# Optimization experiments

Measured on AMD Instinct MI355X. Metric: run time of the kernel, lower is better.

The kernel has to match this reference:

```python
import jax, jax.numpy as jnp
import numpy as np

S = 72
IMG_W, IMG_H = 640, 360
STRIDE = 32
FMAP_H, FMAP_W = IMG_H // STRIDE, IMG_W // STRIDE  # 11, 20
N_OFFSETS = S
N_STRIPS = S - 1
ANGLES = np.array([15.0, 22.0, 30.0, 39.0, 49.0, 60.0, 72.0, 80.0, 90.0, 100.0, 108.0, 120.0, 131.0, 141.0, 150.0, 158.0, 165.0])
N_ANG = 17
N_PRED = 2 + 2 + 1 + N_OFFSETS  # 77
N_EDGE = FMAP_W + 2 * FMAP_H    # 42
N_PROP = N_ANG * N_EDGE         # 714
NMS_THRES = 15.0
BACKBONE_C = 512
CONV_C = 1024


def _make_anchors():
    anchor_ys = np.linspace(1.0, 0.0, N_OFFSETS)
    tan = np.tan(np.deg2rad(ANGLES))
    def side(origins):
        out = np.zeros((N_ANG, N_PRED, len(origins)), np.float32)
        for i, (sx, sy) in enumerate(origins):
            out[:, 2, i] = 1.0 - sy
            out[:, 3, i] = sx
            out[:, 5:, i] = (sx + (sy - anchor_ys)[None, :] / tan[:, None]) * IMG_W
        return out.reshape(N_ANG * N_PRED, len(origins))
    left = side([(0.0, y) for y in np.linspace(1.0, 0.0, FMAP_H)])
    right = side([(1.0, y) for y in np.linspace(1.0, 0.0, FMAP_H)])
    bottom = side([(x, 1.0) for x in np.linspace(1.0, 0.0, FMAP_W)])
    anchors = np.zeros((N_ANG * N_PRED, FMAP_H, FMAP_W), np.float32)
    anchors[:, :, 0] = left
    anchors[:, :, -1] = right
    anchors[:, -1, :] = bottom
    edge = np.concatenate([anchors[:, :, 0], anchors[:, :, -1], anchors[:, -1, :]], 1)  # [1309,42]
    anch_dim = edge.reshape(N_ANG, N_PRED, N_EDGE).transpose(2, 0, 1).reshape(N_PROP, N_PRED)
    return jnp.asarray(anchors), jnp.asarray(anch_dim)


def setup_inputs():
    key = jax.random.key(0)
    ks = jax.random.split(key, 4)
    B = 32
    feat = jax.random.normal(ks[0], (B, BACKBONE_C, FMAP_H, FMAP_W), jnp.float32)
    W_conv = jax.random.normal(ks[1], (CONV_C, BACKBONE_C), jnp.float32) * 0.02
    b_conv = jnp.zeros((CONV_C,), jnp.float32)
    W_cls = jax.random.normal(ks[2], (2 * N_ANG, CONV_C), jnp.float32) * 0.02
    b_cls = jnp.zeros((2 * N_ANG,), jnp.float32)
    W_reg = jax.random.normal(ks[3], (N_ANG * (N_OFFSETS + 1), CONV_C), jnp.float32) * 0.02
    b_reg = jnp.zeros((N_ANG * (N_OFFSETS + 1),), jnp.float32)
    anchors, anchors_anchor_dim = _make_anchors()
    return {"feat": feat, "W_conv": W_conv, "b_conv": b_conv, "W_cls": W_cls, "b_cls": b_cls,
            "W_reg": W_reg, "b_reg": b_reg, "anchors": anchors, "anchors_anchor_dim": anchors_anchor_dim}


def _proposals(feat, W_conv, b_conv, W_cls, b_cls, W_reg, b_reg, anchors):
    B = feat.shape[0]
    features = jnp.einsum('bchw,oc->bohw', feat, W_conv) + b_conv[None, :, None, None]
    cls_f = jnp.einsum('bchw,oc->bohw', features, W_cls) + b_cls[None, :, None, None]
    reg_f = jnp.einsum('bchw,oc->bohw', features, W_reg) + b_reg[None, :, None, None]
    anch = anchors.reshape(N_ANG, N_PRED, FMAP_H, FMAP_W)
    cls_r = cls_f.reshape(B, N_ANG, 2, FMAP_H, FMAP_W)
    reg_r = reg_f.reshape(B, N_ANG, N_OFFSETS + 1, FMAP_H, FMAP_W)
    # slots 0:2 <- cls logits (set), slots 2:4 <- anchor (copied), slots 4: <- anchor + reg
    mid = jnp.broadcast_to(anch[None, :, 2:4], (B, N_ANG, 2, FMAP_H, FMAP_W))
    tail = anch[None, :, 4:] + reg_r
    lane = jnp.concatenate([cls_r, mid, tail], axis=2)  # [B,17,77,h,w]
    # gather the three feature-map edges: left col, right col, bottom row
    edges = jnp.concatenate([lane[:, :, :, :, 0], lane[:, :, :, :, -1], lane[:, :, :, -1, :]], axis=3)  # [B,17,77,42]
    return edges.transpose(0, 3, 1, 2).reshape(B, N_PROP, N_PRED)  # [B,714,77]


def _nms_one(props, scores):
    # greedy line-NMS over proposals of one image, shapes static
    order = jnp.argsort(-scores)
    p = props[order]
    start = jnp.clip(jnp.round(p[:, 2] * N_STRIPS), 0.0, float(N_STRIPS))
    end = jnp.clip(start + p[:, 4] - 1.0, 0.0, float(N_STRIPS))
    xs = p[:, 5:]  # [N,72]
    s = jnp.maximum(start[:, None], start[None, :])
    e = jnp.minimum(end[:, None], end[None, :])
    idx = jnp.arange(N_OFFSETS, dtype=p.dtype)
    m = (idx[None, None, :] >= s[..., None]) & (idx[None, None, :] <= e[..., None])  # [N,N,72]
    diff = jnp.abs(xs[:, None, :] - xs[None, :, :])  # [N,N,72]
    cnt = e - s + 1.0
    dist = jnp.where(cnt > 0, jnp.sum(diff * m, -1) / jnp.maximum(cnt, 1.0), jnp.inf)
    sup = dist < NMS_THRES
    n = p.shape[0]
    pos = jnp.arange(n)
    def step(suppressed, i):
        keep_i = ~suppressed[i]
        suppressed = suppressed | (keep_i & sup[i] & (pos > i))
        return suppressed, keep_i
    _, keep_sorted = jax.lax.scan(step, jnp.zeros(n, bool), pos)
    return jnp.zeros(n, bool).at[order].set(keep_sorted)


def reference(feat, W_conv, b_conv, W_cls, b_cls, W_reg, b_reg, anchors, anchors_anchor_dim):
    proposals = _proposals(feat, W_conv, b_conv, W_cls, b_cls, W_reg, b_reg, anchors)
    scores = jax.nn.softmax(proposals[..., :2], axis=-1)[..., 1]  # [B,714]
    keep_mask = jax.lax.map(lambda pr: _nms_one(pr[0], pr[1]), (proposals, scores))  # [B,714]
    return proposals, keep_mask, scores
```

## Files before the change

kernel.cpp:

```cpp
#include <hip/hip_runtime.h>
#include <math.h>

#define NB     32
#define FH     11
#define FW     20
#define CIN    512
#define CMID   1024
#define NANG   17
#define NPREDD 77
#define NEDGE  42
#define NPROPP 714
#define NOFF   72
#define NCLS   34
#define NREGR  1241
#define N2PAD  1280
#define MTOT   1344
#define NSTRIPSF 71.0f
#define PADK   40

typedef unsigned long long u64;
typedef unsigned short ushortt;
typedef short s8v __attribute__((ext_vector_type(8)));
typedef ushortt u4v __attribute__((ext_vector_type(4)));
typedef float f4v __attribute__((ext_vector_type(4)));

__device__ inline ushortt f2bf(float f) {
    unsigned u = __float_as_uint(f);
    u += 0x7fffu + ((u >> 16) & 1u);
    return (ushortt)(u >> 16);
}
__device__ inline float bf2f(ushortt h) {
    return __uint_as_float(((unsigned)h) << 16);
}

__global__ __launch_bounds__(256) void k_prep(const float* __restrict__ feat,
                                              ushortt* __restrict__ A1hi,
                                              ushortt* __restrict__ A1lo,
                                              const float* __restrict__ Wconv,
                                              ushortt* __restrict__ B1h,
                                              ushortt* __restrict__ B1l,
                                              const float* __restrict__ Wcls,
                                              const float* __restrict__ Wreg,
                                              ushortt* __restrict__ B2h,
                                              ushortt* __restrict__ B2l)
{
    __shared__ unsigned T[32 * 221];
    int bid = blockIdx.x, tid = threadIdx.x;
    if (bid < 512) {
        int p0 = bid * 32;
        int b  = p0 >> 9;
        int c0 = p0 & 511;
        const float* fp = feat + (size_t)p0 * 220;
        for (int i = tid; i < 32 * 220; i += 256) {
            float v = fp[i];
            int pl = i / 220, off = i - pl * 220;
            ushortt hi = f2bf(v);
            ushortt lo = f2bf(v - bf2f(hi));
            T[pl * 221 + off] = ((unsigned)hi) | (((unsigned)lo) << 16);
        }
        __syncthreads();
        int cl = tid & 31;
        for (int e = tid >> 5; e < NEDGE; e += 8) {
            int hw = (e < FH) ? e * FW
                   : (e < 2 * FH) ? (e - FH) * FW + (FW - 1)
                   : (FH - 1) * FW + (e - 2 * FH);
            unsigned u = T[cl * 221 + hw];
            size_t o = (size_t)(b * NEDGE + e) * CIN + c0 + cl;
            A1hi[o] = (ushortt)(u & 0xffffu);
            A1lo[o] = (ushortt)(u >> 16);
        }
    } else if (bid < 1024) {
        int t = (bid - 512) * 256 + tid;
        float4 v = *(const float4*)(Wconv + (size_t)t * 4);
        float vf[4] = {v.x, v.y, v.z, v.w};
        u4v hv, lv;
#pragma unroll
        for (int j = 0; j < 4; ++j) {
            ushortt h = f2bf(vf[j]);
            hv[j] = h;
            lv[j] = f2bf(vf[j] - bf2f(h));
        }
        *(u4v*)(B1h + (size_t)t * 4) = hv;
        *(u4v*)(B1l + (size_t)t * 4) = lv;
    } else {
        int t = (bid - 1024) * 256 + tid;
        int row = t >> 8, col = (t & 255) * 4;
        float4 v = make_float4(0.f, 0.f, 0.f, 0.f);
        if (row < NCLS)              v = *(const float4*)(Wcls + (size_t)row * CMID + col);
        else if (row < NCLS + NREGR) v = *(const float4*)(Wreg + (size_t)(row - NCLS) * CMID + col);
        float vf[4] = {v.x, v.y, v.z, v.w};
        u4v hv, lv;
#pragma unroll
        for (int j = 0; j < 4; ++j) {
            ushortt h = f2bf(vf[j]);
            hv[j] = h;
            lv[j] = f2bf(vf[j] - bf2f(h));
        }
        *(u4v*)(B2h + (size_t)t * 4) = hv;
        *(u4v*)(B2l + (size_t)t * 4) = lv;
    }
}

__global__ __launch_bounds__(256) void k_gemm1m(const ushortt* __restrict__ Ahi,
                                                const ushortt* __restrict__ Alo,
                                                const ushortt* __restrict__ Bh,
                                                const ushortt* __restrict__ Bl,
                                                const float* __restrict__ bias,
                                                ushortt* __restrict__ Chi,
                                                ushortt* __restrict__ Clo)
{
    const int K = CIN, N = CMID;
    __shared__ __align__(16) ushortt Ash[2][64 * PADK], Asl[2][64 * PADK];
    __shared__ __align__(16) ushortt Bsh[2][64 * PADK], Bsl[2][64 * PADK];
    int tid = threadIdx.x;
    int m0 = blockIdx.y * 64, n0 = blockIdx.x * 64;
    int srow = tid >> 2, sg = tid & 3;
    int lane = tid & 63, wv = tid >> 6;
    int wm = (wv & 1) * 32, wn = (wv >> 1) * 32;
    int quad = lane >> 4, l15 = lane & 15;
    int wo = srow * PADK + sg * 8;

    f4v acc[2][2];
#pragma unroll
    for (int i = 0; i < 2; ++i)
#pragma unroll
        for (int j = 0; j < 2; ++j) acc[i][j] = (f4v){0.f, 0.f, 0.f, 0.f};

    const ushortt* Ahp = Ahi + (size_t)(m0 + srow) * K + sg * 8;
    const ushortt* Alp = Alo + (size_t)(m0 + srow) * K + sg * 8;
    const ushortt* Bhp = Bh  + (size_t)(n0 + srow) * K + sg * 8;
    const ushortt* Blp = Bl  + (size_t)(n0 + srow) * K + sg * 8;

    s8v ra = *(const s8v*)Ahp;
    s8v rl = *(const s8v*)Alp;
    s8v rb = *(const s8v*)Bhp;
    s8v rc = *(const s8v*)Blp;
    *(s8v*)&Ash[0][wo] = ra;
    *(s8v*)&Asl[0][wo] = rl;
    *(s8v*)&Bsh[0][wo] = rb;
    *(s8v*)&Bsl[0][wo] = rc;
    __syncthreads();

    int buf = 0;
    for (int k0 = 0; k0 < K; k0 += 32) {
        bool more = (k0 + 32 < K);
        if (more) {
            ra = *(const s8v*)(Ahp + k0 + 32);
            rl = *(const s8v*)(Alp + k0 + 32);
            rb = *(const s8v*)(Bhp + k0 + 32);
            rc = *(const s8v*)(Blp + k0 + 32);
        }
        s8v ah[2], al[2], bh[2], bl[2];
#pragma unroll
        for (int s = 0; s < 2; ++s) {
            ah[s] = *(const s8v*)&Ash[buf][(wm + s * 16 + l15) * PADK + quad * 8];
            al[s] = *(const s8v*)&Asl[buf][(wm + s * 16 + l15) * PADK + quad * 8];
            bh[s] = *(const s8v*)&Bsh[buf][(wn + s * 16 + l15) * PADK + quad * 8];
            bl[s] = *(const s8v*)&Bsl[buf][(wn + s * 16 + l15) * PADK + quad * 8];
        }
#pragma unroll
        for (int sm = 0; sm < 2; ++sm)
#pragma unroll
            for (int sn = 0; sn < 2; ++sn) {
                acc[sm][sn] = __builtin_amdgcn_mfma_f32_16x16x32_bf16(al[sm], bl[sn], acc[sm][sn], 0, 0, 0);
                acc[sm][sn] = __builtin_amdgcn_mfma_f32_16x16x32_bf16(al[sm], bh[sn], acc[sm][sn], 0, 0, 0);
                acc[sm][sn] = __builtin_amdgcn_mfma_f32_16x16x32_bf16(ah[sm], bl[sn], acc[sm][sn], 0, 0, 0);
                acc[sm][sn] = __builtin_amdgcn_mfma_f32_16x16x32_bf16(ah[sm], bh[sn], acc[sm][sn], 0, 0, 0);
            }
        if (more) {
            *(s8v*)&Ash[buf ^ 1][wo] = ra;
            *(s8v*)&Asl[buf ^ 1][wo] = rl;
            *(s8v*)&Bsh[buf ^ 1][wo] = rb;
            *(s8v*)&Bsl[buf ^ 1][wo] = rc;
        }
        __syncthreads();
        buf ^= 1;
    }
#pragma unroll
    for (int sm = 0; sm < 2; ++sm)
#pragma unroll
        for (int sn = 0; sn < 2; ++sn)
#pragma unroll
            for (int r = 0; r < 4; ++r) {
                int m = m0 + wm + sm * 16 + quad * 4 + r;
                int n = n0 + wn + sn * 16 + l15;
                float v = acc[sm][sn][r] + bias[n];
                ushortt h = f2bf(v);
                Chi[(size_t)m * N + n] = h;
                Clo[(size_t)m * N + n] = f2bf(v - bf2f(h));
            }
}

__global__ __launch_bounds__(256) void k_gemm2m(const ushortt* __restrict__ Ahi,
                                                const ushortt* __restrict__ Alo,
                                                const ushortt* __restrict__ Bh,
                                                const ushortt* __restrict__ Bl,
                                                const float* __restrict__ bcls,
                                                const float* __restrict__ breg,
                                                float* __restrict__ C)
{
    const int K = CMID;
    __shared__ __align__(16) ushortt Ash[2][64 * PADK], Asl[2][64 * PADK];
    __shared__ __align__(16) ushortt Bsh[2][64 * PADK], Bsl[2][64 * PADK];
    int tid = threadIdx.x;
    int m0 = blockIdx.y * 64, n0 = blockIdx.x * 64;
    int srow = tid >> 2, sg = tid & 3;
    int lane = tid & 63, wv = tid >> 6;
    int wm = (wv & 1) * 32, wn = (wv >> 1) * 32;
    int quad = lane >> 4, l15 = lane & 15;
    int wo = srow * PADK + sg * 8;

    f4v acc[2][2];
#pragma unroll
    for (int i = 0; i < 2; ++i)
#pragma unroll
        for (int j = 0; j < 2; ++j) acc[i][j] = (f4v){0.f, 0.f, 0.f, 0.f};

    const ushortt* Ahp = Ahi + (size_t)(m0 + srow) * K + sg * 8;
    const ushortt* Alp = Alo + (size_t)(m0 + srow) * K + sg * 8;
    const ushortt* Bhp = Bh  + (size_t)(n0 + srow) * K + sg * 8;
    const ushortt* Blp = Bl  + (size_t)(n0 + srow) * K + sg * 8;

    s8v ra = *(const s8v*)Ahp;
    s8v rl = *(const s8v*)Alp;
    s8v rb = *(const s8v*)Bhp;
    s8v rc = *(const s8v*)Blp;
    *(s8v*)&Ash[0][wo] = ra;
    *(s8v*)&Asl[0][wo] = rl;
    *(s8v*)&Bsh[0][wo] = rb;
    *(s8v*)&Bsl[0][wo] = rc;
    __syncthreads();

    int buf = 0;
    for (int k0 = 0; k0 < K; k0 += 32) {
        bool more = (k0 + 32 < K);
        if (more) {
            ra = *(const s8v*)(Ahp + k0 + 32);
            rl = *(const s8v*)(Alp + k0 + 32);
            rb = *(const s8v*)(Bhp + k0 + 32);
            rc = *(const s8v*)(Blp + k0 + 32);
        }
        s8v ah[2], al[2], bh[2], bl[2];
#pragma unroll
        for (int s = 0; s < 2; ++s) {
            ah[s] = *(const s8v*)&Ash[buf][(wm + s * 16 + l15) * PADK + quad * 8];
            al[s] = *(const s8v*)&Asl[buf][(wm + s * 16 + l15) * PADK + quad * 8];
            bh[s] = *(const s8v*)&Bsh[buf][(wn + s * 16 + l15) * PADK + quad * 8];
            bl[s] = *(const s8v*)&Bsl[buf][(wn + s * 16 + l15) * PADK + quad * 8];
        }
#pragma unroll
        for (int sm = 0; sm < 2; ++sm)
#pragma unroll
            for (int sn = 0; sn < 2; ++sn) {
                acc[sm][sn] = __builtin_amdgcn_mfma_f32_16x16x32_bf16(al[sm], bl[sn], acc[sm][sn], 0, 0, 0);
                acc[sm][sn] = __builtin_amdgcn_mfma_f32_16x16x32_bf16(al[sm], bh[sn], acc[sm][sn], 0, 0, 0);
                acc[sm][sn] = __builtin_amdgcn_mfma_f32_16x16x32_bf16(ah[sm], bl[sn], acc[sm][sn], 0, 0, 0);
                acc[sm][sn] = __builtin_amdgcn_mfma_f32_16x16x32_bf16(ah[sm], bh[sn], acc[sm][sn], 0, 0, 0);
            }
        if (more) {
            *(s8v*)&Ash[buf ^ 1][wo] = ra;
            *(s8v*)&Asl[buf ^ 1][wo] = rl;
            *(s8v*)&Bsh[buf ^ 1][wo] = rb;
            *(s8v*)&Bsl[buf ^ 1][wo] = rc;
        }
        __syncthreads();
        buf ^= 1;
    }
#pragma unroll
    for (int sm = 0; sm < 2; ++sm)
#pragma unroll
        for (int sn = 0; sn < 2; ++sn)
#pragma unroll
            for (int r = 0; r < 4; ++r) {
                int m = m0 + wm + sm * 16 + quad * 4 + r;
                int n = n0 + wn + sn * 16 + l15;
                float bb = (n < NCLS) ? bcls[n] : ((n < NCLS + NREGR) ? breg[n - NCLS] : 0.f);
                C[(size_t)m * N2PAD + n] = acc[sm][sn][r] + bb;
            }
}

__global__ __launch_bounds__(256) void k_assemble(const float* __restrict__ C2,
                                                  const float* __restrict__ AD,
                                                  float* __restrict__ outP,
                                                  float* __restrict__ outS,
                                                  float* __restrict__ startv,
                                                  float* __restrict__ endv,
                                                  float* __restrict__ xsel)
{
    int mb = blockIdx.x;
    int b = mb / NEDGE, e = mb - b * NEDGE;
    const float* c2 = C2 + (size_t)mb * N2PAD;
    int tid = threadIdx.x;
    for (int idx = tid; idx < NANG * NPREDD; idx += 256) {
        int a = idx / NPREDD, p = idx - a * NPREDD;
        int prop = e * NANG + a;
        float v;
        if (p < 2) v = c2[a * 2 + p];
        else {
            v = AD[prop * NPREDD + p];
            if (p >= 4) v += c2[NCLS + a * 73 + (p - 4)];
        }
        outP[((size_t)b * NPROPP + prop) * NPREDD + p] = v;
    }
    if (tid < NANG) {
        int a = tid, prop = e * NANG + a;
        float c0 = c2[2 * a], c1 = c2[2 * a + 1];
        float mx = fmaxf(c0, c1);
        float e0 = expf(c0 - mx), e1 = expf(c1 - mx);
        outS[b * NPROPP + prop] = e1 / (e0 + e1);
        float p2 = AD[prop * NPREDD + 2];
        float p4 = AD[prop * NPREDD + 4] + c2[NCLS + a * 73];
        float st = fminf(fmaxf(rintf(p2 * NSTRIPSF), 0.0f), NSTRIPSF);
        float en = fminf(fmaxf(st + p4 - 1.0f, 0.0f), NSTRIPSF);
        startv[b * 720 + prop] = st;
        endv[b * 720 + prop] = en;
        int ksi = (int)st;
        xsel[b * 720 + prop] = AD[prop * NPREDD + 5 + ksi] + c2[NCLS + a * 73 + ksi + 1];
    }
}

__global__ __launch_bounds__(128) void k_sort(const float* __restrict__ scores,
                                              int* __restrict__ order)
{
    int b = blockIdx.x, tile = blockIdx.y, tid = threadIdx.x;
    __shared__ __align__(16) float s[720];
    for (int x = tid; x < 720; x += 128)
        s[x] = (x < NPROPP) ? scores[b * NPROPP + x] : -1e30f;
    __syncthreads();
    int i = tile * 128 + tid;
    if (i >= NPROPP) return;
    float si = s[i];
    int r = 0;
#pragma unroll 4
    for (int j4 = 0; j4 < 720; j4 += 4) {
        float4 v = *(const float4*)&s[j4];
        r += (v.x > si) || (v.x == si && (j4 + 0) < i);
        r += (v.y > si) || (v.y == si && (j4 + 1) < i);
        r += (v.z > si) || (v.z == si && (j4 + 2) < i);
        r += (v.w > si) || (v.w == si && (j4 + 3) < i);
    }
    order[b * 720 + r] = i;
}

__global__ __launch_bounds__(256) void k_supmat(const float* __restrict__ outP,
                                                const float* __restrict__ startv,
                                                const float* __restrict__ endv,
                                                const float* __restrict__ xsel,
                                                const int* __restrict__ order,
                                                u64* __restrict__ sup)
{
    int jt = blockIdx.x, it = blockIdx.y, b = blockIdx.z;
    int i0 = it * 64, j0 = jt * 64;
    int tid = threadIdx.x;
    if (j0 + 63 < i0) {
        if (tid < 64) {
            int il = i0 + tid;
            if (il < NPROPP) sup[((size_t)b * NPROPP + il) * 12 + jt] = 0ull;
        }
        return;
    }
    __shared__ float SI[64], EI[64], XI[64];
    __shared__ float SJ[64], EJ[64], XJ[64];
    __shared__ int   OI[64], OJ[64];
    if (tid < 128) {
        int side = tid >> 6, q = tid & 63;
        int pos = (side ? j0 : i0) + q;
        int o = (pos < NPROPP) ? order[b * 720 + pos] : -1;
        float st = (o >= 0) ? startv[b * 720 + o] : 0.f;
        float en = (o >= 0) ? endv[b * 720 + o] : -2.f;
        float xv = (o >= 0) ? xsel[b * 720 + o] : 0.f;
        if (!side) { SI[q] = st; EI[q] = en; XI[q] = xv; OI[q] = o; }
        else       { SJ[q] = st; EJ[q] = en; XJ[q] = xv; OJ[q] = o; }
    }
    __syncthreads();
    int lane = tid & 63, w = tid >> 6;
    int j = j0 + lane;
    float sj = SJ[lane], ej = EJ[lane], xj = XJ[lane];
    const float* basexs = outP + (size_t)b * NPROPP * NPREDD + 5;
#pragma unroll 1
    for (int rep = 0; rep < 16; ++rep) {
        int iloc = w * 16 + rep;
        int il = i0 + iloc;
        float si = SI[iloc], ei = EI[iloc];
        float s = fmaxf(si, sj), e = fminf(ei, ej);
        float cnt = e - s + 1.0f;
        bool sp = false;
        if (cnt > 0.f) {
            if (e < s) {
                sp = true;
            } else {
                int ks = (int)s, ke = (int)e;
                if (si == sj && ke == ks) {
                    sp = (fabsf(XI[iloc] - xj) / fmaxf(cnt, 1.0f)) < 15.0f;
                } else {
                    const float* xi  = basexs + (size_t)OI[iloc] * NPREDD;
                    const float* xjp = basexs + (size_t)OJ[lane] * NPREDD;
                    float sum = 0.f;
                    for (int k = ks; k <= ke; ++k)
                        sum += fabsf(xi[k] - xjp[k]);
                    sp = (sum / fmaxf(cnt, 1.0f)) < 15.0f;
                }
            }
        }
        bool valid = (il < NPROPP) && (j < NPROPP) && (j > il);
        u64 msk = __ballot(valid && sp);
        if (lane == 0 && il < NPROPP)
            sup[((size_t)b * NPROPP + il) * 12 + jt] = msk;
    }
}

__global__ __launch_bounds__(256) void k_scan(const u64* __restrict__ sup,
                                              const int* __restrict__ order,
                                              float* __restrict__ keep_out)
{
    int b = blockIdx.x, tid = threadIdx.x;
    int lane = tid & 63;
    __shared__ u64 K[12], NS[12];
    __shared__ int changed;
    const u64* base = sup + (size_t)b * NPROPP * 12;

    int r0 = tid, r1 = tid + 256, r2 = tid + 512;
    u64 row0[12], row1[12], row2[12];
#pragma unroll
    for (int t = 0; t < 12; ++t) {
        row0[t] = base[(size_t)r0 * 12 + t];
        row1[t] = (r1 < NPROPP) ? base[(size_t)r1 * 12 + t] : 0ull;
        row2[t] = (r2 < NPROPP) ? base[(size_t)r2 * 12 + t] : 0ull;
    }
    if (tid < 12) {
        K[tid] = (tid < 11) ? ~0ull : ((1ull << (NPROPP - 704)) - 1ull);
        NS[tid] = 0ull;
    }
    __syncthreads();

    for (int sweep = 0; sweep < 720; ++sweep) {
        u64 m0 = 0ull - ((K[r0 >> 6] >> (r0 & 63)) & 1ull);
        u64 m1 = (r1 < NPROPP) ? (0ull - ((K[r1 >> 6] >> (r1 & 63)) & 1ull)) : 0ull;
        u64 m2 = (r2 < NPROPP) ? (0ull - ((K[r2 >> 6] >> (r2 & 63)) & 1ull)) : 0ull;
        unsigned lo[12], hi[12];
#pragma unroll
        for (int t = 0; t < 12; ++t) {
            u64 a = (row0[t] & m0) | (row1[t] & m1) | (row2[t] & m2);
            lo[t] = (unsigned)a;
            hi[t] = (unsigned)(a >> 32);
        }
#pragma unroll
        for (int s = 1; s < 64; s <<= 1) {
#pragma unroll
            for (int t = 0; t < 12; ++t) {
                lo[t] |= __shfl_xor(lo[t], s, 64);
                hi[t] |= __shfl_xor(hi[t], s, 64);
            }
        }
        if (tid == 0) changed = 0;
        if (lane == 0) {
#pragma unroll
            for (int t = 0; t < 12; ++t)
                atomicOr(&NS[t], ((u64)hi[t] << 32) | (u64)lo[t]);
        }
        __syncthreads();
        if (tid < 12) {
            u64 valid = (tid < 11) ? ~0ull : ((1ull << (NPROPP - 704)) - 1ull);
            u64 nk = valid & ~NS[tid];
            if (nk != K[tid]) changed = 1;
            K[tid] = nk;
            NS[tid] = 0ull;
        }
        __syncthreads();
        if (!changed) break;
    }
    if (r0 < NPROPP)
        keep_out[b * NPROPP + order[b * 720 + r0]] =
            ((K[r0 >> 6] >> (r0 & 63)) & 1ull) ? 1.f : 0.f;
    if (r1 < NPROPP)
        keep_out[b * NPROPP + order[b * 720 + r1]] =
            ((K[r1 >> 6] >> (r1 & 63)) & 1ull) ? 1.f : 0.f;
    if (r2 < NPROPP)
        keep_out[b * NPROPP + order[b * 720 + r2]] =
            ((K[r2 >> 6] >> (r2 & 63)) & 1ull) ? 1.f : 0.f;
}

extern "C" void kernel_launch(void* const* d_in, const int* in_sizes, int n_in,
                              void* d_out, int out_size, void* d_ws, size_t ws_size,
                              hipStream_t stream)
{
    const float* feat  = (const float*)d_in[0];
    const float* Wconv = (const float*)d_in[1];
    const float* bconv = (const float*)d_in[2];
    const float* Wcls  = (const float*)d_in[3];
    const float* bcls  = (const float*)d_in[4];
    const float* Wreg  = (const float*)d_in[5];
    const float* breg  = (const float*)d_in[6];
    const float* AD    = (const float*)d_in[8];

    float* out  = (float*)d_out;
    float* outP = out;
    float* outK = out + (size_t)NB * NPROPP * NPREDD;
    float* outS = outK + (size_t)NB * NPROPP;

    float* ws = (float*)d_ws;
    ushortt* A1hi = (ushortt*)ws;
    ushortt* A1lo = (ushortt*)(ws + 344064);
    ushortt* A2hi = (ushortt*)(ws + 688128);
    ushortt* A2lo = (ushortt*)(ws + 1376256);
    float*   C2   = ws + 2064384;
    ushortt* B1h  = (ushortt*)(ws + 3784704);
    ushortt* B1l  = (ushortt*)(ws + 4046848);
    ushortt* B2h  = (ushortt*)(ws + 4308992);
    ushortt* B2l  = (ushortt*)(ws + 4964352);
    float* startv = ws;
    float* endv   = ws + 23040;
    int*   order  = (int*)(ws + 46080);
    u64*   sup    = (u64*)(ws + 69120);
    float* xsel   = ws + 617472;

    k_prep        <<<dim3(2304),       dim3(256), 0, stream>>>(feat, A1hi, A1lo,
                                                               Wconv, B1h, B1l,
                                                               Wcls, Wreg, B2h, B2l);
    k_gemm1m      <<<dim3(16, 21),     dim3(256), 0, stream>>>(A1hi, A1lo, B1h, B1l, bconv, A2hi, A2lo);
    k_gemm2m      <<<dim3(20, 21),     dim3(256), 0, stream>>>(A2hi, A2lo, B2h, B2l, bcls, breg, C2);
    k_assemble    <<<dim3(MTOT),       dim3(256), 0, stream>>>(C2, AD, outP, outS, startv, endv, xsel);
    k_sort        <<<dim3(NB, 6),      dim3(128), 0, stream>>>(outS, order);
    k_supmat      <<<dim3(12, 12, NB), dim3(256), 0, stream>>>(outP, startv, endv, xsel, order, sup);
    k_scan        <<<dim3(NB),         dim3(256), 0, stream>>>(sup, order, outK);
}
```

Baseline: 184.8 us.

## Unroll GEMM pipeline by two, launch only upper-triangular suppression tiles

Both bf16-split GEMM kernels now unroll the K loop by two, using two register sets with statically indexed LDS buffers. This is meant to cut index arithmetic and let the global prefetch run further ahead. The suppression-matrix kernel launches only the 78 upper-triangular tile pairs per batch instead of 144 and returns early for none. The scan kernel now treats the skipped lower tiles as zero instead of reading them, which keeps results correct.

```diff
diff --git a/kernel.cpp b/kernel.cpp
--- a/kernel.cpp
+++ b/kernel.cpp
@@ -101,6 +101,39 @@
     }
 }
 
+#define GEMM_STEP(BUF)                                                               \
+    {                                                                                \
+        s8v ah[2], al[2], bh[2], bl[2];                                              \
+        _Pragma("unroll")                                                            \
+        for (int s = 0; s < 2; ++s) {                                                \
+            ah[s] = *(const s8v*)&Ash[BUF][(wm + s * 16 + l15) * PADK + quad * 8];   \
+            al[s] = *(const s8v*)&Asl[BUF][(wm + s * 16 + l15) * PADK + quad * 8];   \
+            bh[s] = *(const s8v*)&Bsh[BUF][(wn + s * 16 + l15) * PADK + quad * 8];   \
+            bl[s] = *(const s8v*)&Bsl[BUF][(wn + s * 16 + l15) * PADK + quad * 8];   \
+        }                                                                            \
+        _Pragma("unroll")                                                            \
+        for (int sm = 0; sm < 2; ++sm)                                               \
+            _Pragma("unroll")                                                        \
+            for (int sn = 0; sn < 2; ++sn) {                                         \
+                acc[sm][sn] = __builtin_amdgcn_mfma_f32_16x16x32_bf16(al[sm], bl[sn], acc[sm][sn], 0, 0, 0); \
+                acc[sm][sn] = __builtin_amdgcn_mfma_f32_16x16x32_bf16(al[sm], bh[sn], acc[sm][sn], 0, 0, 0); \
+                acc[sm][sn] = __builtin_amdgcn_mfma_f32_16x16x32_bf16(ah[sm], bl[sn], acc[sm][sn], 0, 0, 0); \
+                acc[sm][sn] = __builtin_amdgcn_mfma_f32_16x16x32_bf16(ah[sm], bh[sn], acc[sm][sn], 0, 0, 0); \
+            }                                                                        \
+    }
+
+#define LOADSET(dst_a, dst_l, dst_b, dst_c, OFF)                                     \
+    dst_a = *(const s8v*)(Ahp + (OFF));                                              \
+    dst_l = *(const s8v*)(Alp + (OFF));                                              \
+    dst_b = *(const s8v*)(Bhp + (OFF));                                              \
+    dst_c = *(const s8v*)(Blp + (OFF));
+
+#define WRITESET(src_a, src_l, src_b, src_c, BUF)                                    \
+    *(s8v*)&Ash[BUF][wo] = src_a;                                                    \
+    *(s8v*)&Asl[BUF][wo] = src_l;                                                    \
+    *(s8v*)&Bsh[BUF][wo] = src_b;                                                    \
+    *(s8v*)&Bsl[BUF][wo] = src_c;
+
 __global__ __launch_bounds__(256) void k_gemm1m(const ushortt* __restrict__ Ahi,
                                                 const ushortt* __restrict__ Alo,
                                                 const ushortt* __restrict__ Bh,
@@ -110,6 +143,7 @@
                                                 ushortt* __restrict__ Clo)
 {
     const int K = CIN, N = CMID;
+    const int NT = K / 32;
     __shared__ __align__(16) ushortt Ash[2][64 * PADK], Asl[2][64 * PADK];
     __shared__ __align__(16) ushortt Bsh[2][64 * PADK], Bsl[2][64 * PADK];
     int tid = threadIdx.x;
@@ -131,50 +165,21 @@
     const ushortt* Bhp = Bh  + (size_t)(n0 + srow) * K + sg * 8;
     const ushortt* Blp = Bl  + (size_t)(n0 + srow) * K + sg * 8;
 
-    s8v ra = *(const s8v*)Ahp;
-    s8v rl = *(const s8v*)Alp;
-    s8v rb = *(const s8v*)Bhp;
-    s8v rc = *(const s8v*)Blp;
-    *(s8v*)&Ash[0][wo] = ra;
-    *(s8v*)&Asl[0][wo] = rl;
-    *(s8v*)&Bsh[0][wo] = rb;
-    *(s8v*)&Bsl[0][wo] = rc;
+    s8v a0, l0, b0, c0, a1, l1, b1, c1;
+    LOADSET(a0, l0, b0, c0, 0)
+    WRITESET(a0, l0, b0, c0, 0)
+    LOADSET(a1, l1, b1, c1, 32)
     __syncthreads();
 
-    int buf = 0;
-    for (int k0 = 0; k0 < K; k0 += 32) {
-        bool more = (k0 + 32 < K);
-        if (more) {
-            ra = *(const s8v*)(Ahp + k0 + 32);
-            rl = *(const s8v*)(Alp + k0 + 32);
-            rb = *(const s8v*)(Bhp + k0 + 32);
-            rc = *(const s8v*)(Blp + k0 + 32);
-        }
-        s8v ah[2], al[2], bh[2], bl[2];
-#pragma unroll
-        for (int s = 0; s < 2; ++s) {
-            ah[s] = *(const s8v*)&Ash[buf][(wm + s * 16 + l15) * PADK + quad * 8];
-            al[s] = *(const s8v*)&Asl[buf][(wm + s * 16 + l15) * PADK + quad * 8];
-            bh[s] = *(const s8v*)&Bsh[buf][(wn + s * 16 + l15) * PADK + quad * 8];
-            bl[s] = *(const s8v*)&Bsl[buf][(wn + s * 16 + l15) * PADK + quad * 8];
-        }
-#pragma unroll
-        for (int sm = 0; sm < 2; ++sm)
-#pragma unroll
-            for (int sn = 0; sn < 2; ++sn) {
-                acc[sm][sn] = __builtin_amdgcn_mfma_f32_16x16x32_bf16(al[sm], bl[sn], acc[sm][sn], 0, 0, 0);
-                acc[sm][sn] = __builtin_amdgcn_mfma_f32_16x16x32_bf16(al[sm], bh[sn], acc[sm][sn], 0, 0, 0);
-                acc[sm][sn] = __builtin_amdgcn_mfma_f32_16x16x32_bf16(ah[sm], bl[sn], acc[sm][sn], 0, 0, 0);
-                acc[sm][sn] = __builtin_amdgcn_mfma_f32_16x16x32_bf16(ah[sm], bh[sn], acc[sm][sn], 0, 0, 0);
-            }
-        if (more) {
-            *(s8v*)&Ash[buf ^ 1][wo] = ra;
-            *(s8v*)&Asl[buf ^ 1][wo] = rl;
-            *(s8v*)&Bsh[buf ^ 1][wo] = rb;
-            *(s8v*)&Bsl[buf ^ 1][wo] = rc;
-        }
-        __syncthreads();
-        buf ^= 1;
+    for (int k = 0; k < NT; k += 2) {
+        if (k + 2 < NT) { LOADSET(a0, l0, b0, c0, (k + 2) * 32) }
+        GEMM_STEP(0)
+        WRITESET(a1, l1, b1, c1, 1)
+        __syncthreads();
+        if (k + 3 < NT) { LOADSET(a1, l1, b1, c1, (k + 3) * 32) }
+        GEMM_STEP(1)
+        if (k + 2 < NT) { WRITESET(a0, l0, b0, c0, 0) }
+        __syncthreads();
     }
 #pragma unroll
     for (int sm = 0; sm < 2; ++sm)
@@ -200,6 +205,7 @@
                                                 float* __restrict__ C)
 {
     const int K = CMID;
+    const int NT = K / 32;
     __shared__ __align__(16) ushortt Ash[2][64 * PADK], Asl[2][64 * PADK];
     __shared__ __align__(16) ushortt Bsh[2][64 * PADK], Bsl[2][64 * PADK];
     int tid = threadIdx.x;
@@ -221,50 +227,21 @@
     const ushortt* Bhp = Bh  + (size_t)(n0 + srow) * K + sg * 8;
     const ushortt* Blp = Bl  + (size_t)(n0 + srow) * K + sg * 8;
 
-    s8v ra = *(const s8v*)Ahp;
-    s8v rl = *(const s8v*)Alp;
-    s8v rb = *(const s8v*)Bhp;
-    s8v rc = *(const s8v*)Blp;
-    *(s8v*)&Ash[0][wo] = ra;
-    *(s8v*)&Asl[0][wo] = rl;
-    *(s8v*)&Bsh[0][wo] = rb;
-    *(s8v*)&Bsl[0][wo] = rc;
+    s8v a0, l0, b0, c0, a1, l1, b1, c1;
+    LOADSET(a0, l0, b0, c0, 0)
+    WRITESET(a0, l0, b0, c0, 0)
+    LOADSET(a1, l1, b1, c1, 32)
     __syncthreads();
 
-    int buf = 0;
-    for (int k0 = 0; k0 < K; k0 += 32) {
-        bool more = (k0 + 32 < K);
-        if (more) {
-            ra = *(const s8v*)(Ahp + k0 + 32);
-            rl = *(const s8v*)(Alp + k0 + 32);
-            rb = *(const s8v*)(Bhp + k0 + 32);
-            rc = *(const s8v*)(Blp + k0 + 32);
-        }
-        s8v ah[2], al[2], bh[2], bl[2];
-#pragma unroll
-        for (int s = 0; s < 2; ++s) {
-            ah[s] = *(const s8v*)&Ash[buf][(wm + s * 16 + l15) * PADK + quad * 8];
-            al[s] = *(const s8v*)&Asl[buf][(wm + s * 16 + l15) * PADK + quad * 8];
-            bh[s] = *(const s8v*)&Bsh[buf][(wn + s * 16 + l15) * PADK + quad * 8];
-            bl[s] = *(const s8v*)&Bsl[buf][(wn + s * 16 + l15) * PADK + quad * 8];
-        }
-#pragma unroll
-        for (int sm = 0; sm < 2; ++sm)
-#pragma unroll
-            for (int sn = 0; sn < 2; ++sn) {
-                acc[sm][sn] = __builtin_amdgcn_mfma_f32_16x16x32_bf16(al[sm], bl[sn], acc[sm][sn], 0, 0, 0);
-                acc[sm][sn] = __builtin_amdgcn_mfma_f32_16x16x32_bf16(al[sm], bh[sn], acc[sm][sn], 0, 0, 0);
-                acc[sm][sn] = __builtin_amdgcn_mfma_f32_16x16x32_bf16(ah[sm], bl[sn], acc[sm][sn], 0, 0, 0);
-                acc[sm][sn] = __builtin_amdgcn_mfma_f32_16x16x32_bf16(ah[sm], bh[sn], acc[sm][sn], 0, 0, 0);
-            }
-        if (more) {
-            *(s8v*)&Ash[buf ^ 1][wo] = ra;
-            *(s8v*)&Asl[buf ^ 1][wo] = rl;
-            *(s8v*)&Bsh[buf ^ 1][wo] = rb;
-            *(s8v*)&Bsl[buf ^ 1][wo] = rc;
-        }
-        __syncthreads();
-        buf ^= 1;
+    for (int k = 0; k < NT; k += 2) {
+        if (k + 2 < NT) { LOADSET(a0, l0, b0, c0, (k + 2) * 32) }
+        GEMM_STEP(0)
+        WRITESET(a1, l1, b1, c1, 1)
+        __syncthreads();
+        if (k + 3 < NT) { LOADSET(a1, l1, b1, c1, (k + 3) * 32) }
+        GEMM_STEP(1)
+        if (k + 2 < NT) { WRITESET(a0, l0, b0, c0, 0) }
+        __syncthreads();
     }
 #pragma unroll
     for (int sm = 0; sm < 2; ++sm)
@@ -349,16 +326,12 @@
                                                 const int* __restrict__ order,
                                                 u64* __restrict__ sup)
 {
-    int jt = blockIdx.x, it = blockIdx.y, b = blockIdx.z;
+    int u = blockIdx.x, b = blockIdx.y;
+    int it = 0, rem = 12;
+    while (u >= rem) { u -= rem; --rem; ++it; }
+    int jt = it + u;
     int i0 = it * 64, j0 = jt * 64;
     int tid = threadIdx.x;
-    if (j0 + 63 < i0) {
-        if (tid < 64) {
-            int il = i0 + tid;
-            if (il < NPROPP) sup[((size_t)b * NPROPP + il) * 12 + jt] = 0ull;
-        }
-        return;
-    }
     __shared__ float SI[64], EI[64], XI[64];
     __shared__ float SJ[64], EJ[64], XJ[64];
     __shared__ int   OI[64], OJ[64];
@@ -420,12 +393,13 @@
     const u64* base = sup + (size_t)b * NPROPP * 12;
 
     int r0 = tid, r1 = tid + 256, r2 = tid + 512;
+    int t0 = r0 >> 6, t1 = r1 >> 6, t2 = r2 >> 6;
     u64 row0[12], row1[12], row2[12];
 #pragma unroll
     for (int t = 0; t < 12; ++t) {
-        row0[t] = base[(size_t)r0 * 12 + t];
-        row1[t] = (r1 < NPROPP) ? base[(size_t)r1 * 12 + t] : 0ull;
-        row2[t] = (r2 < NPROPP) ? base[(size_t)r2 * 12 + t] : 0ull;
+        row0[t] = (t >= t0) ? base[(size_t)r0 * 12 + t] : 0ull;
+        row1[t] = (r1 < NPROPP && t >= t1) ? base[(size_t)r1 * 12 + t] : 0ull;
+        row2[t] = (r2 < NPROPP && t >= t2) ? base[(size_t)r2 * 12 + t] : 0ull;
     }
     if (tid < 12) {
         K[tid] = (tid < 11) ? ~0ull : ((1ull << (NPROPP - 704)) - 1ull);
@@ -521,6 +495,6 @@
     k_gemm2m      <<<dim3(20, 21),     dim3(256), 0, stream>>>(A2hi, A2lo, B2h, B2l, bcls, breg, C2);
     k_assemble    <<<dim3(MTOT),       dim3(256), 0, stream>>>(C2, AD, outP, outS, startv, endv, xsel);
     k_sort        <<<dim3(NB, 6),      dim3(128), 0, stream>>>(outS, order);
-    k_supmat      <<<dim3(12, 12, NB), dim3(256), 0, stream>>>(outP, startv, endv, xsel, order, sup);
+    k_supmat      <<<dim3(78, NB),     dim3(256), 0, stream>>>(outP, startv, endv, xsel, order, sup);
     k_scan        <<<dim3(NB),         dim3(256), 0, stream>>>(sup, order, outK);
 }
```

After: 174.4 us, median of 2. 1.06x faster.
